# Kernel optimization log

Hardware: AMD Instinct MI355X
Metric: run time of the kernel (lower is better)

Reference implementation:

```python
import jax, jax.numpy as jnp
import numpy as np
from jax import lax

N = 2048
B = 8
CH = 10
START = 1
STOP = 65


def setup_inputs() -> dict:
    key = jax.random.key(0)
    ks = jax.random.split(key, 13)

    def g(k, s):
        return jax.random.normal(k, s, jnp.float32) * 0.05

    return {
        "x": jax.random.normal(ks[0], (B, 1, N, N), jnp.float32),
        "wl": g(ks[1], (CH // 2, 1, 3, N)), "bl": g(ks[2], (CH // 2,)),
        "wr": g(ks[3], (CH // 2, 1, N, 3)), "br": g(ks[4], (CH // 2,)),
        "wA": g(ks[5], (CH, CH, 3)), "bA": g(ks[6], (CH,)),
        "wB": g(ks[7], (CH, CH, 3)), "bB": g(ks[8], (CH,)),  # shared by layers 2&3 (torch list aliasing)
        "wT": g(ks[9], (CH, CH, 3)), "bT": g(ks[10], (CH,)),
        "wm": g(ks[11], (2, CH, 1)), "bm": g(ks[12], (2,)),
        "start": START, "stop": STOP,
    }


def _conv1d(h, w, b, pad):
    y = lax.conv_general_dilated(h, w, (1,), [(pad, pad)], dimension_numbers=("NCH", "OIH", "NCH"))
    return y + b[None, :, None]


def _forward(x, wl, bl, wr, br, wA, bA, wB, bB, wT, bT, wm, bm, start, stop):
    n = x.shape[-1]
    # scan_left: Conv2d kernel (3, n), padding (1, 0) -> (B, 5, n, 1) -> squeeze
    left_ = lax.conv_general_dilated(x, wl, (1, 1), [(1, 1), (0, 0)], dimension_numbers=("NCHW", "OIHW", "NCHW"))
    left_ = left_[..., 0] + bl[None, :, None]
    # scan_right: Conv2d kernel (n, 3), padding (0, 1) -> (B, 5, 1, n) -> squeeze
    right_ = lax.conv_general_dilated(x, wr, (1, 1), [(0, 0), (1, 1)], dimension_numbers=("NCHW", "OIHW", "NCHW"))
    right_ = right_[:, :, 0, :] + br[None, :, None]
    lr = jnp.concatenate([left_, right_], axis=1)  # (B, 10, n)
    h = jax.nn.relu(_conv1d(lr, wA, bA, 1))
    h = jax.nn.relu(_conv1d(h, wB, bB, 1))  # same weights twice: torch [conv, relu]*2 aliasing
    h = jax.nn.relu(_conv1d(h, wB, bB, 1))
    # ConvTranspose1d(k=3, stride=1, pad=1) == Conv1d with transposed, spatially-flipped kernel, pad=1
    wTc = jnp.flip(jnp.swapaxes(wT, 0, 1), -1)
    for _ in range(3):
        h = jax.nn.relu(_conv1d(h, wTc, bT, 1))
    m = jax.nn.sigmoid(_conv1d(h, wm, bm, 0))  # (B, 2, n)
    left, right = m[:, 0, :], m[:, 1, :]
    xs = x[:, 0]  # (B, n, n)
    preds = []
    for d in range(start, stop):  # static diagonal indices
        curr = jnp.exp(jnp.diagonal(xs, offset=d, axis1=1, axis2=2))  # (B, n-d)
        mass_in = curr[:, 1:] * right[:, 1:n - d] + curr[:, :-1] * left[:, d:n - 1]
        mass_out = right[:, 0:n - d - 1] + left[:, d + 1:n]
        p = jnp.log(mass_in / mass_out)
        preds.append(p - jnp.mean(p))  # scalar mean over batch+positions, as torch.mean
    return jnp.concatenate(preds, axis=1)  # ragged preds concatenated: (B, sum(n-d-1))


def reference(x, wl, bl, wr, br, wA, bA, wB, bB, wT, bT, wm, bm, start, stop):
    return _forward(x, wl, bl, wr, br, wA, bA, wB, bB, wT, bT, wm, bm, start, stop)
```

## Files before the change

### kernel.cpp

```cpp
#include <hip/hip_runtime.h>

#define NN 2048
#define BB 8
#define TROW 128928

typedef __attribute__((ext_vector_type(8))) short bf16x8;
typedef __attribute__((ext_vector_type(4))) float f32x4;

__device__ __forceinline__ short f2bf(float f) {
    unsigned u = __float_as_uint(f);
    unsigned r = (u + 0x7FFFu + ((u >> 16) & 1u)) >> 16;
    return (short)r;
}

__global__ __launch_bounds__(256) void k_stage1(const float* __restrict__ x,
                                                const float* __restrict__ wl,
                                                const float* __restrict__ wr,
                                                float* __restrict__ R,
                                                float* __restrict__ CSp,
                                                float* __restrict__ psum,
                                                int* __restrict__ counters) {
    int blk = blockIdx.x;
    int tid = threadIdx.x;
    if (blk == 0) {
        if (tid < 64) psum[tid] = 0.f;
        else if (tid < 66) counters[tid - 64] = 0;
    }
    if (blk < 256) {
        int b = blk >> 5;
        int rg = blk & 31;
        int wv = tid >> 6, lane = tid & 63;
        int q = lane >> 4, m = lane & 15;
        int r0 = rg * 64 + wv * 16;
        int nrow = (m == 15) ? 14 : m;

        const float* ap = x + ((size_t)(b * NN + r0 + m)) * NN + q * 8;
        const float* bp = wl + (size_t)nrow * NN + q * 8;

        f32x4 acc = {0.f, 0.f, 0.f, 0.f};
#pragma unroll 4
        for (int it = 0; it < 64; it++) {
            const float* a0 = ap + it * 32;
            const float* b0 = bp + it * 32;
            float4 av0 = *(const float4*)(a0);
            float4 av1 = *(const float4*)(a0 + 4);
            float4 bv0 = *(const float4*)(b0);
            float4 bv1 = *(const float4*)(b0 + 4);
            bf16x8 af, bf;
            af[0] = f2bf(av0.x); af[1] = f2bf(av0.y); af[2] = f2bf(av0.z); af[3] = f2bf(av0.w);
            af[4] = f2bf(av1.x); af[5] = f2bf(av1.y); af[6] = f2bf(av1.z); af[7] = f2bf(av1.w);
            bf[0] = f2bf(bv0.x); bf[1] = f2bf(bv0.y); bf[2] = f2bf(bv0.z); bf[3] = f2bf(bv0.w);
            bf[4] = f2bf(bv1.x); bf[5] = f2bf(bv1.y); bf[6] = f2bf(bv1.z); bf[7] = f2bf(bv1.w);
            acc = __builtin_amdgcn_mfma_f32_16x16x32_bf16(af, bf, acc, 0, 0, 0);
        }
        float* rp = R + ((size_t)b * NN + r0) * 16;
#pragma unroll
        for (int reg = 0; reg < 4; reg++)
            rp[(q * 4 + reg) * 16 + m] = acc[reg];
    } else {
        int blk2 = blk - 256;
        int b = blk2 >> 5;
        int rem = blk2 & 31;
        int jc = rem >> 4, rc = rem & 15;
        int r0 = rc * 128;
        int c0 = jc * 1024 + tid * 4;
        const float* xp = x + ((size_t)b * NN + r0) * NN + c0;

        float acc[15][4];
#pragma unroll
        for (int k = 0; k < 15; k++)
#pragma unroll
            for (int e = 0; e < 4; e++) acc[k][e] = 0.f;

        for (int rb = 0; rb < 16; rb++) {
            float4 xv[8];
#pragma unroll
            for (int q = 0; q < 8; q++)
                xv[q] = *(const float4*)(xp + (size_t)(rb * 8 + q) * NN);
#pragma unroll
            for (int q = 0; q < 8; q++) {
                int h = r0 + rb * 8 + q;
#pragma unroll
                for (int k = 0; k < 15; k++) {
                    int c = k / 3, dw = k - c * 3;
                    float wk = wr[c * (NN * 3) + h * 3 + dw];
                    acc[k][0] = fmaf(xv[q].x, wk, acc[k][0]);
                    acc[k][1] = fmaf(xv[q].y, wk, acc[k][1]);
                    acc[k][2] = fmaf(xv[q].z, wk, acc[k][2]);
                    acc[k][3] = fmaf(xv[q].w, wk, acc[k][3]);
                }
            }
        }
        float* outp = CSp + ((size_t)(rc * BB + b) * 16) * NN + c0;
#pragma unroll
        for (int k = 0; k < 15; k++) {
            float4 v; v.x = acc[k][0]; v.y = acc[k][1]; v.z = acc[k][2]; v.w = acc[k][3];
            *(float4*)(outp + (size_t)k * NN) = v;
        }
    }
}

__global__ __launch_bounds__(256) void k_rest(const float* __restrict__ x,
                                              const float* __restrict__ R,
                                              const float* __restrict__ CSp,
                                              const float* __restrict__ bl,
                                              const float* __restrict__ br,
                                              const float* __restrict__ wA, const float* __restrict__ bA,
                                              const float* __restrict__ wB, const float* __restrict__ bB,
                                              const float* __restrict__ wT, const float* __restrict__ bT,
                                              const float* __restrict__ wm, const float* __restrict__ bm,
                                              float* __restrict__ LEFT, float* __restrict__ RIGHT,
                                              float* __restrict__ psum,
                                              int* __restrict__ counters,
                                              float* __restrict__ outp) {
    __shared__ float T[65][65];
    __shared__ float buf0[10][80], buf1[10][80];
    __shared__ float W[3][10][10][3];
    __shared__ float Bs[3][10];
    __shared__ float Wm[2][10], Bm[2];
    __shared__ float psl[64];
    __shared__ float lfs[132], rts[68];

    int b = blockIdx.x >> 5;
    int t5 = blockIdx.x & 31;
    int c0 = t5 << 6;
    int i0 = t5 << 6;
    int tid = threadIdx.x;

    for (int idx = tid; idx < 65 * 64; idx += 256) {
        int r = idx >> 6, dm1 = idx & 63;
        int row = i0 + r;
        int col = row + dm1 + 1;
        float v = 0.f;
        if (row < NN && col < NN) v = __expf(x[((size_t)b * NN + row) * NN + col]);
        T[r][dm1] = v;
    }

    for (int idx = tid; idx < 900; idx += 256) {
        int set = idx / 300, rem = idx - set * 300;
        int o = rem / 30, rem2 = rem - o * 30, c = rem2 / 3, kk = rem2 - c * 3;
        float u;
        if (set == 0) u = wA[o * 30 + c * 3 + kk];
        else if (set == 1) u = wB[o * 30 + c * 3 + kk];
        else u = wT[c * 30 + o * 3 + (2 - kk)];
        W[set][o][c][kk] = u;
    }
    if (tid < 30) {
        float v = (tid < 10) ? bA[tid] : (tid < 20) ? bB[tid - 10] : bT[tid - 20];
        Bs[tid / 10][tid % 10] = v;
    }
    if (tid < 20) Wm[tid / 10][tid % 10] = wm[tid];
    if (tid < 2) Bm[tid] = bm[tid];

    for (int idx = tid; idx < 760; idx += 256) {
        int ch = idx / 76, p = idx - ch * 76;
        int g = c0 - 6 + p;
        float v = 0.f;
        if (g >= 0 && g < NN) {
            if (ch < 5) {
                v = bl[ch];
#pragma unroll
                for (int dh = 0; dh < 3; dh++) {
                    int r = g + dh - 1;
                    if (r >= 0 && r < NN) v += R[(size_t)(b * NN + r) * 16 + ch * 3 + dh];
                }
            } else {
                int c = ch - 5;
                v = br[c];
#pragma unroll
                for (int dw = 0; dw < 3; dw++) {
                    int j = g + dw - 1;
                    if (j >= 0 && j < NN) {
                        const float* csp = CSp + ((size_t)(b * 16) + c * 3 + dw) * NN + j;
#pragma unroll
                        for (int rc = 0; rc < 16; rc++)
                            v += csp[(size_t)rc * (8 * 16 * NN)];
                    }
                }
            }
        }
        buf0[ch][p] = v;
    }
    __syncthreads();

    float(*in)[80] = buf0;
    float(*out)[80] = buf1;
    for (int layer = 0; layer < 6; layer++) {
        int set = (layer == 0) ? 0 : (layer < 3 ? 1 : 2);
        int lo = layer + 1;
        for (int idx = tid; idx < 760; idx += 256) {
            int o = idx / 76, p = idx - o * 76;
            if (p >= lo && p < 76 - lo) {
                float s = Bs[set][o];
#pragma unroll
                for (int c = 0; c < 10; c++) {
                    const float* ip = &in[c][p];
                    s = fmaf(ip[-1], W[set][o][c][0], s);
                    s = fmaf(ip[0], W[set][o][c][1], s);
                    s = fmaf(ip[1], W[set][o][c][2], s);
                }
                s = s > 0.f ? s : 0.f;
                int g = c0 - 6 + p;
                if (g < 0 || g >= NN) s = 0.f;
                out[o][p] = s;
            }
        }
        __syncthreads();
        float(*tmp)[80] = in; in = out; out = tmp;
    }
    if (tid < 128) {
        int o = tid >> 6, pp = tid & 63;
        int p = 6 + pp;
        float s = Bm[o];
#pragma unroll
        for (int c = 0; c < 10; c++) s = fmaf(in[c][p], Wm[o][c], s);
        float sig = 1.f / (1.f + __expf(-s));
        float* dst = (o ? RIGHT : LEFT) + b * NN + c0 + pp;
        __hip_atomic_store(dst, sig, __ATOMIC_RELAXED, __HIP_MEMORY_SCOPE_AGENT);
    }
    __syncthreads();

    if (tid == 0) {
        __threadfence();
        atomicAdd(&counters[0], 1);
        while (__hip_atomic_load(&counters[0], __ATOMIC_ACQUIRE, __HIP_MEMORY_SCOPE_AGENT) < 256) {
            __builtin_amdgcn_s_sleep(2);
        }
    }
    __syncthreads();

    if (tid < 195) {
        if (tid < 129) {
            int g = i0 + 1 + tid; if (g > NN - 1) g = NN - 1;
            lfs[tid] = __hip_atomic_load(LEFT + b * NN + g, __ATOMIC_RELAXED, __HIP_MEMORY_SCOPE_AGENT);
        } else {
            int p2 = tid - 129;
            int g = i0 + p2; if (g > NN - 1) g = NN - 1;
            rts[p2] = __hip_atomic_load(RIGHT + b * NN + g, __ATOMIC_RELAXED, __HIP_MEMORY_SCOPE_AGENT);
        }
    }
    __syncthreads();

    int wv = tid >> 6, lane = tid & 63;
    int i = i0 + lane;
    float pv[16];
#pragma unroll
    for (int s = 0; s < 16; s++) {
        int dm1 = wv * 16 + s;
        int d = dm1 + 1;
        int L = (NN - 1) - d;
        float p = 0.f;
        if (i < L) {
            float mi = T[lane + 1][dm1] * rts[lane + 1] + T[lane][dm1] * lfs[dm1 + lane];
            float mo = rts[lane] + lfs[dm1 + lane + 1];
            p = __logf(mi / mo);
        }
        pv[s] = p;
        float s64 = p;
        for (int off = 32; off; off >>= 1) s64 += __shfl_down(s64, off);
        if (lane == 0) psl[dm1] = s64;
    }
    __syncthreads();
    if (tid < 64) atomicAdd(&psum[tid], psl[tid]);
    __syncthreads();

    if (tid == 0) {
        __threadfence();
        atomicAdd(&counters[1], 1);
        while (__hip_atomic_load(&counters[1], __ATOMIC_ACQUIRE, __HIP_MEMORY_SCOPE_AGENT) < 256) {
            __builtin_amdgcn_s_sleep(2);
        }
    }
    __syncthreads();
    if (tid < 64)
        psl[tid] = __hip_atomic_load(&psum[tid], __ATOMIC_RELAXED, __HIP_MEMORY_SCOPE_AGENT);
    __syncthreads();

#pragma unroll
    for (int s = 0; s < 16; s++) {
        int dm1 = wv * 16 + s;
        int d = dm1 + 1;
        int L = (NN - 1) - d;
        if (i < L) {
            float mean = psl[dm1] / (float)(8 * L);
            size_t off0 = (size_t)dm1 * (NN - 1) - (size_t)dm1 * (dm1 + 1) / 2;
            outp[(size_t)b * TROW + off0 + i] = pv[s] - mean;
        }
    }
}

extern "C" void kernel_launch(void* const* d_in, const int* in_sizes, int n_in,
                              void* d_out, int out_size, void* d_ws, size_t ws_size,
                              hipStream_t stream) {
    const float* x = (const float*)d_in[0];
    const float* wl = (const float*)d_in[1];
    const float* bl = (const float*)d_in[2];
    const float* wr = (const float*)d_in[3];
    const float* br = (const float*)d_in[4];
    const float* wA = (const float*)d_in[5];
    const float* bA = (const float*)d_in[6];
    const float* wB = (const float*)d_in[7];
    const float* bB = (const float*)d_in[8];
    const float* wT = (const float*)d_in[9];
    const float* bT = (const float*)d_in[10];
    const float* wm = (const float*)d_in[11];
    const float* bm = (const float*)d_in[12];

    float* ws = (float*)d_ws;
    float* R     = ws;
    float* CSp   = ws + 262144;
    float* LEFT  = ws + 4456448;
    float* RIGHT = ws + 4472832;
    float* psum  = ws + 4489216;
    int*   counters = (int*)(ws + 4489280);

    k_stage1<<<512, 256, 0, stream>>>(x, wl, wr, R, CSp, psum, counters);
    k_rest<<<256, 256, 0, stream>>>(x, R, CSp, bl, br, wA, bA, wB, bB, wT, bT, wm, bm,
                                    LEFT, RIGHT, psum, counters, (float*)d_out);
}
```

Before: 288.8 us.

## Fuse stage1 and rest into one persistent kernel with atomic column-sum reduction

Merges the two kernels into one 512-thread kernel. Half of each block runs the MFMA row reduction and the other half the column partial sums. The column partials are reduced into CS with atomicAdd instead of being written out per row-chunk and summed by the consumer, and a grid-wide counter barrier replaces the kernel boundary. The T tile exp and weight loads now overlap the wait on that barrier. It also switches bf16 conversion to packed intrinsics and adds a memset of the accumulators. In exchange it adds float atomics contention and relies on all 256 blocks being co-resident for the spin barriers.

Result: slower. 330.8 us (+14.5%).

```diff
diff --git a/kernel.cpp b/kernel.cpp
--- a/kernel.cpp
+++ b/kernel.cpp
@@ -1,34 +1,51 @@
 #include <hip/hip_runtime.h>
+#include <hip/hip_bf16.h>
 
 #define NN 2048
 #define BB 8
 #define TROW 128928
 
 typedef __attribute__((ext_vector_type(8))) short bf16x8;
+typedef __attribute__((ext_vector_type(4))) unsigned u32x4;
 typedef __attribute__((ext_vector_type(4))) float f32x4;
 
-__device__ __forceinline__ short f2bf(float f) {
-    unsigned u = __float_as_uint(f);
-    unsigned r = (u + 0x7FFFu + ((u >> 16) & 1u)) >> 16;
-    return (short)r;
+__device__ __forceinline__ unsigned pk2(float lo, float hi) {
+    float2 t; t.x = lo; t.y = hi;
+    __hip_bfloat162 h = __float22bfloat162_rn(t);
+    union { __hip_bfloat162 h; unsigned u; } c; c.h = h;
+    return c.u;
 }
 
-__global__ __launch_bounds__(256) void k_stage1(const float* __restrict__ x,
+__global__ __launch_bounds__(512, 2) void k_all(const float* __restrict__ x,
                                                 const float* __restrict__ wl,
                                                 const float* __restrict__ wr,
+                                                const float* __restrict__ bl,
+                                                const float* __restrict__ br,
+                                                const float* __restrict__ wA, const float* __restrict__ bA,
+                                                const float* __restrict__ wB, const float* __restrict__ bB,
+                                                const float* __restrict__ wT, const float* __restrict__ bT,
+                                                const float* __restrict__ wm, const float* __restrict__ bm,
                                                 float* __restrict__ R,
-                                                float* __restrict__ CSp,
+                                                float* __restrict__ CS,
+                                                float* __restrict__ LEFT, float* __restrict__ RIGHT,
                                                 float* __restrict__ psum,
-                                                int* __restrict__ counters) {
+                                                int* __restrict__ counters,
+                                                float* __restrict__ outp) {
+    __shared__ float T[65][65];
+    __shared__ float buf0[10][80], buf1[10][80];
+    __shared__ float W[3][10][10][3];
+    __shared__ float Bs[3][10];
+    __shared__ float Wm[2][10], Bm[2];
+    __shared__ float psl[64];
+    __shared__ float lfs[132], rts[68];
+
     int blk = blockIdx.x;
     int tid = threadIdx.x;
-    if (blk == 0) {
-        if (tid < 64) psum[tid] = 0.f;
-        else if (tid < 66) counters[tid - 64] = 0;
-    }
-    if (blk < 256) {
-        int b = blk >> 5;
-        int rg = blk & 31;
+    int b = blk >> 5;
+    int rg = blk & 31;
+    int i0 = rg << 6;
+
+    if (tid < 256) {
         int wv = tid >> 6, lane = tid & 63;
         int q = lane >> 4, m = lane & 15;
         int r0 = rg * 64 + wv * 16;
@@ -46,24 +63,22 @@
             float4 av1 = *(const float4*)(a0 + 4);
             float4 bv0 = *(const float4*)(b0);
             float4 bv1 = *(const float4*)(b0 + 4);
-            bf16x8 af, bf;
-            af[0] = f2bf(av0.x); af[1] = f2bf(av0.y); af[2] = f2bf(av0.z); af[3] = f2bf(av0.w);
-            af[4] = f2bf(av1.x); af[5] = f2bf(av1.y); af[6] = f2bf(av1.z); af[7] = f2bf(av1.w);
-            bf[0] = f2bf(bv0.x); bf[1] = f2bf(bv0.y); bf[2] = f2bf(bv0.z); bf[3] = f2bf(bv0.w);
-            bf[4] = f2bf(bv1.x); bf[5] = f2bf(bv1.y); bf[6] = f2bf(bv1.z); bf[7] = f2bf(bv1.w);
-            acc = __builtin_amdgcn_mfma_f32_16x16x32_bf16(af, bf, acc, 0, 0, 0);
+            union { bf16x8 v; u32x4 u; } A, Bv;
+            A.u[0] = pk2(av0.x, av0.y); A.u[1] = pk2(av0.z, av0.w);
+            A.u[2] = pk2(av1.x, av1.y); A.u[3] = pk2(av1.z, av1.w);
+            Bv.u[0] = pk2(bv0.x, bv0.y); Bv.u[1] = pk2(bv0.z, bv0.w);
+            Bv.u[2] = pk2(bv1.x, bv1.y); Bv.u[3] = pk2(bv1.z, bv1.w);
+            acc = __builtin_amdgcn_mfma_f32_16x16x32_bf16(A.v, Bv.v, acc, 0, 0, 0);
         }
         float* rp = R + ((size_t)b * NN + r0) * 16;
 #pragma unroll
         for (int reg = 0; reg < 4; reg++)
             rp[(q * 4 + reg) * 16 + m] = acc[reg];
     } else {
-        int blk2 = blk - 256;
-        int b = blk2 >> 5;
-        int rem = blk2 & 31;
-        int jc = rem >> 4, rc = rem & 15;
+        int t2 = tid - 256;
+        int jc = rg >> 4, rc = rg & 15;
         int r0 = rc * 128;
-        int c0 = jc * 1024 + tid * 4;
+        int c0 = jc * 1024 + t2 * 4;
         const float* xp = x + ((size_t)b * NN + r0) * NN + c0;
 
         float acc[15][4];
@@ -91,52 +106,22 @@
                 }
             }
         }
-        float* outp = CSp + ((size_t)(rc * BB + b) * 16) * NN + c0;
 #pragma unroll
         for (int k = 0; k < 15; k++) {
-            float4 v; v.x = acc[k][0]; v.y = acc[k][1]; v.z = acc[k][2]; v.w = acc[k][3];
-            *(float4*)(outp + (size_t)k * NN) = v;
-        }
-    }
-}
-
-__global__ __launch_bounds__(256) void k_rest(const float* __restrict__ x,
-                                              const float* __restrict__ R,
-                                              const float* __restrict__ CSp,
-                                              const float* __restrict__ bl,
-                                              const float* __restrict__ br,
-                                              const float* __restrict__ wA, const float* __restrict__ bA,
-                                              const float* __restrict__ wB, const float* __restrict__ bB,
-                                              const float* __restrict__ wT, const float* __restrict__ bT,
-                                              const float* __restrict__ wm, const float* __restrict__ bm,
-                                              float* __restrict__ LEFT, float* __restrict__ RIGHT,
-                                              float* __restrict__ psum,
-                                              int* __restrict__ counters,
-                                              float* __restrict__ outp) {
-    __shared__ float T[65][65];
-    __shared__ float buf0[10][80], buf1[10][80];
-    __shared__ float W[3][10][10][3];
-    __shared__ float Bs[3][10];
-    __shared__ float Wm[2][10], Bm[2];
-    __shared__ float psl[64];
-    __shared__ float lfs[132], rts[68];
-
-    int b = blockIdx.x >> 5;
-    int t5 = blockIdx.x & 31;
-    int c0 = t5 << 6;
-    int i0 = t5 << 6;
-    int tid = threadIdx.x;
-
-    for (int idx = tid; idx < 65 * 64; idx += 256) {
-        int r = idx >> 6, dm1 = idx & 63;
-        int row = i0 + r;
-        int col = row + dm1 + 1;
-        float v = 0.f;
-        if (row < NN && col < NN) v = __expf(x[((size_t)b * NN + row) * NN + col]);
-        T[r][dm1] = v;
-    }
-
-    for (int idx = tid; idx < 900; idx += 256) {
+            float* dst = CS + ((size_t)b * 16 + k) * NN + c0;
+            atomicAdd(dst + 0, acc[k][0]);
+            atomicAdd(dst + 1, acc[k][1]);
+            atomicAdd(dst + 2, acc[k][2]);
+            atomicAdd(dst + 3, acc[k][3]);
+        }
+    }
+    __syncthreads();
+    if (tid == 0) {
+        __threadfence();
+        atomicAdd(&counters[0], 1);
+    }
+
+    for (int idx = tid; idx < 900; idx += 512) {
         int set = idx / 300, rem = idx - set * 300;
         int o = rem / 30, rem2 = rem - o * 30, c = rem2 / 3, kk = rem2 - c * 3;
         float u;
@@ -152,9 +137,25 @@
     if (tid < 20) Wm[tid / 10][tid % 10] = wm[tid];
     if (tid < 2) Bm[tid] = bm[tid];
 
-    for (int idx = tid; idx < 760; idx += 256) {
+    for (int idx = tid; idx < 65 * 64; idx += 512) {
+        int r = idx >> 6, dm1 = idx & 63;
+        int row = i0 + r;
+        int col = row + dm1 + 1;
+        float v = 0.f;
+        if (row < NN && col < NN) v = __expf(x[((size_t)b * NN + row) * NN + col]);
+        T[r][dm1] = v;
+    }
+
+    if (tid == 0) {
+        while (__hip_atomic_load(&counters[0], __ATOMIC_ACQUIRE, __HIP_MEMORY_SCOPE_AGENT) < 256) {
+            __builtin_amdgcn_s_sleep(2);
+        }
+    }
+    __syncthreads();
+
+    for (int idx = tid; idx < 760; idx += 512) {
         int ch = idx / 76, p = idx - ch * 76;
-        int g = c0 - 6 + p;
+        int g = i0 - 6 + p;
         float v = 0.f;
         if (g >= 0 && g < NN) {
             if (ch < 5) {
@@ -162,7 +163,9 @@
 #pragma unroll
                 for (int dh = 0; dh < 3; dh++) {
                     int r = g + dh - 1;
-                    if (r >= 0 && r < NN) v += R[(size_t)(b * NN + r) * 16 + ch * 3 + dh];
+                    if (r >= 0 && r < NN)
+                        v += __hip_atomic_load(&R[(size_t)(b * NN + r) * 16 + ch * 3 + dh],
+                                               __ATOMIC_RELAXED, __HIP_MEMORY_SCOPE_AGENT);
                 }
             } else {
                 int c = ch - 5;
@@ -170,12 +173,9 @@
 #pragma unroll
                 for (int dw = 0; dw < 3; dw++) {
                     int j = g + dw - 1;
-                    if (j >= 0 && j < NN) {
-                        const float* csp = CSp + ((size_t)(b * 16) + c * 3 + dw) * NN + j;
-#pragma unroll
-                        for (int rc = 0; rc < 16; rc++)
-                            v += csp[(size_t)rc * (8 * 16 * NN)];
-                    }
+                    if (j >= 0 && j < NN)
+                        v += __hip_atomic_load(&CS[((size_t)b * 16 + c * 3 + dw) * NN + j],
+                                               __ATOMIC_RELAXED, __HIP_MEMORY_SCOPE_AGENT);
                 }
             }
         }
@@ -188,7 +188,7 @@
     for (int layer = 0; layer < 6; layer++) {
         int set = (layer == 0) ? 0 : (layer < 3 ? 1 : 2);
         int lo = layer + 1;
-        for (int idx = tid; idx < 760; idx += 256) {
+        for (int idx = tid; idx < 760; idx += 512) {
             int o = idx / 76, p = idx - o * 76;
             if (p >= lo && p < 76 - lo) {
                 float s = Bs[set][o];
@@ -200,7 +200,7 @@
                     s = fmaf(ip[1], W[set][o][c][2], s);
                 }
                 s = s > 0.f ? s : 0.f;
-                int g = c0 - 6 + p;
+                int g = i0 - 6 + p;
                 if (g < 0 || g >= NN) s = 0.f;
                 out[o][p] = s;
             }
@@ -208,6 +208,7 @@
         __syncthreads();
         float(*tmp)[80] = in; in = out; out = tmp;
     }
+
     if (tid < 128) {
         int o = tid >> 6, pp = tid & 63;
         int p = 6 + pp;
@@ -215,15 +216,15 @@
 #pragma unroll
         for (int c = 0; c < 10; c++) s = fmaf(in[c][p], Wm[o][c], s);
         float sig = 1.f / (1.f + __expf(-s));
-        float* dst = (o ? RIGHT : LEFT) + b * NN + c0 + pp;
+        float* dst = (o ? RIGHT : LEFT) + b * NN + i0 + pp;
         __hip_atomic_store(dst, sig, __ATOMIC_RELAXED, __HIP_MEMORY_SCOPE_AGENT);
     }
     __syncthreads();
 
     if (tid == 0) {
         __threadfence();
-        atomicAdd(&counters[0], 1);
-        while (__hip_atomic_load(&counters[0], __ATOMIC_ACQUIRE, __HIP_MEMORY_SCOPE_AGENT) < 256) {
+        atomicAdd(&counters[1], 1);
+        while (__hip_atomic_load(&counters[1], __ATOMIC_ACQUIRE, __HIP_MEMORY_SCOPE_AGENT) < 256) {
             __builtin_amdgcn_s_sleep(2);
         }
     }
@@ -243,10 +244,10 @@
 
     int wv = tid >> 6, lane = tid & 63;
     int i = i0 + lane;
-    float pv[16];
-#pragma unroll
-    for (int s = 0; s < 16; s++) {
-        int dm1 = wv * 16 + s;
+    float pv[8];
+#pragma unroll
+    for (int s = 0; s < 8; s++) {
+        int dm1 = wv * 8 + s;
         int d = dm1 + 1;
         int L = (NN - 1) - d;
         float p = 0.f;
@@ -266,8 +267,8 @@
 
     if (tid == 0) {
         __threadfence();
-        atomicAdd(&counters[1], 1);
-        while (__hip_atomic_load(&counters[1], __ATOMIC_ACQUIRE, __HIP_MEMORY_SCOPE_AGENT) < 256) {
+        atomicAdd(&counters[2], 1);
+        while (__hip_atomic_load(&counters[2], __ATOMIC_ACQUIRE, __HIP_MEMORY_SCOPE_AGENT) < 256) {
             __builtin_amdgcn_s_sleep(2);
         }
     }
@@ -277,8 +278,8 @@
     __syncthreads();
 
 #pragma unroll
-    for (int s = 0; s < 16; s++) {
-        int dm1 = wv * 16 + s;
+    for (int s = 0; s < 8; s++) {
+        int dm1 = wv * 8 + s;
         int d = dm1 + 1;
         int L = (NN - 1) - d;
         if (i < L) {
@@ -308,13 +309,14 @@
 
     float* ws = (float*)d_ws;
     float* R     = ws;
-    float* CSp   = ws + 262144;
-    float* LEFT  = ws + 4456448;
-    float* RIGHT = ws + 4472832;
-    float* psum  = ws + 4489216;
-    int*   counters = (int*)(ws + 4489280);
-
-    k_stage1<<<512, 256, 0, stream>>>(x, wl, wr, R, CSp, psum, counters);
-    k_rest<<<256, 256, 0, stream>>>(x, R, CSp, bl, br, wA, bA, wB, bB, wT, bT, wm, bm,
-                                    LEFT, RIGHT, psum, counters, (float*)d_out);
+    float* LEFT  = ws + 262144;
+    float* RIGHT = ws + 278528;
+    float* CS    = ws + 294912;
+    float* psum  = ws + 557056;
+    int*   counters = (int*)(ws + 557120);
+
+    hipMemsetAsync(ws + 294912, 0, (size_t)(262144 + 64 + 4) * 4, stream);
+
+    k_all<<<256, 512, 0, stream>>>(x, wl, wr, bl, br, wA, bA, wB, bB, wT, bT, wm, bm,
+                                   R, CS, LEFT, RIGHT, psum, counters, (float*)d_out);
 }
```
